# Optimization experiments

Hardware: AMD Instinct MI355X
Metric: run time of the kernel (lower is better)

Reference implementation:

```python
import jax, jax.numpy as jnp
import numpy as np

N_HEAD = 4
N_FEAT = 256
D_K = N_FEAT // N_HEAD


def setup_inputs() -> dict:
    key = jax.random.key(0)
    ks = jax.random.split(key, 7)
    B, T, F = 8, 2048, N_FEAT
    return {
        "query": jax.random.normal(ks[0], (B, T, F), dtype=jnp.float32),
        "key": jax.random.normal(ks[1], (B, T, F), dtype=jnp.float32),
        "value": jax.random.normal(ks[2], (B, T, F), dtype=jnp.float32),
        "mask": jax.random.randint(ks[3], (B, 1, T), 0, 2, dtype=jnp.int32),
        "W_qkv": jax.random.normal(ks[4], (3 * F, 3 * F), dtype=jnp.float32) * 0.02,
        "b_qkv": jnp.zeros((3 * F,), dtype=jnp.float32),
        "W_out": jax.random.normal(ks[5], (F, F), dtype=jnp.float32) * 0.02,
        "b_out": jnp.zeros((F,), dtype=jnp.float32),
    }


def reference(query, key, value, mask, W_qkv, b_qkv, W_out, b_out):
    B, T, F = query.shape
    H, dk = N_HEAD, D_K
    # fused QKV projection on concatenated [q; k; v]  -> (B, T, 3F)
    qkv = jnp.concatenate([query, key, value], axis=-1) @ W_qkv.T + b_qkv
    qkv = qkv.reshape(B, T, H, 3 * dk)
    q, k, v = jnp.split(qkv, 3, axis=-1)          # each (B, T, H, dk)
    q = q.transpose(0, 2, 1, 3)                    # (B, H, T, dk)
    k = k.transpose(0, 2, 1, 3)
    v = v.transpose(0, 2, 1, 3)
    scores = jnp.einsum("bhqd,bhkd->bhqk", q, k) / jnp.sqrt(jnp.float32(dk))
    # mask: (B, 1, T) -> broadcast (B, 1, 1, T); positions where mask==0 are masked
    m = (mask[:, None, :, :] == 0)
    min_val = jnp.finfo(scores.dtype).min
    scores = jnp.where(m, min_val, scores)
    attn = jax.nn.softmax(scores, axis=-1)
    attn = jnp.where(m, jnp.float32(0.0), attn)    # zero masked probs, as in torch code
    x = jnp.einsum("bhqk,bhkd->bhqd", attn, v)     # (B, H, T, dk)
    x = x.transpose(0, 2, 1, 3).reshape(B, T, H * dk)
    return x @ W_out.T + b_out
```

## Files before the change

kernel.cpp:

```cpp
#include <hip/hip_runtime.h>
#include <hip/hip_bf16.h>

#define NB 8
#define NT 2048
#define NH 4
#define NF 256
#define NTF 768
#define NM (NB * NT)

typedef unsigned short u16;
typedef unsigned int u32;
typedef unsigned long long u64;
typedef u16 u16x8 __attribute__((ext_vector_type(8)));
typedef __bf16 bf16x8 __attribute__((ext_vector_type(8)));
typedef float f32x4 __attribute__((ext_vector_type(4)));
typedef float f32x16 __attribute__((ext_vector_type(16)));

__device__ __forceinline__ u16 bf16_rne(float f) {
    union { float f; unsigned u; } x; x.f = f;
    unsigned u = x.u;
    return (u16)((u + 0x7fffu + ((u >> 16) & 1u)) >> 16);
}

__device__ __forceinline__ int swz(int row, int colB) {
    return row * 128 + (colB ^ ((row & 7) << 4));
}

__device__ __forceinline__ void glds16(const void* g, void* l) {
    __builtin_amdgcn_global_load_lds(
        (const __attribute__((address_space(1))) void*)g,
        (__attribute__((address_space(3))) void*)l, 16, 0, 0);
}

__device__ __forceinline__ u32 pkbf16(float lo, float hi) {
    union { __bf16 h2[2]; u32 u; } t;
    t.h2[0] = (__bf16)lo; t.h2[1] = (__bf16)hi;
    return t.u;
}

__device__ __forceinline__ void pl32swap(u32& a, u32& b) {
    asm("v_permlane32_swap_b32 %0, %1" : "+v"(a), "+v"(b));
}

#define mfma32(A, B, C) __builtin_amdgcn_mfma_f32_32x32x16_bf16((A), (B), (C), 0, 0, 0)

__global__ __launch_bounds__(256) void convert_all_kernel(
        const float* __restrict__ q, const float* __restrict__ k,
        const float* __restrict__ v, const float* __restrict__ wqkv,
        const float* __restrict__ wout, const int* __restrict__ mask,
        u16* __restrict__ xcat, u16* __restrict__ wqkvb,
        u16* __restrict__ woutb, float* __restrict__ maskadd) {
    int bid = blockIdx.x;
    if (bid < 6144) {
        int tid = bid * 256 + threadIdx.x;
        int row = tid / 96;
        int c8  = (tid % 96) * 8;
        const float* src; int c;
        if (c8 < NF)            { src = q; c = c8; }
        else if (c8 < 2 * NF)   { src = k; c = c8 - NF; }
        else                    { src = v; c = c8 - 2 * NF; }
        const float4* p = reinterpret_cast<const float4*>(src + (size_t)row * NF + c);
        float4 a = p[0], b = p[1];
        u16x8 o;
        o[0] = bf16_rne(a.x); o[1] = bf16_rne(a.y); o[2] = bf16_rne(a.z); o[3] = bf16_rne(a.w);
        o[4] = bf16_rne(b.x); o[5] = bf16_rne(b.y); o[6] = bf16_rne(b.z); o[7] = bf16_rne(b.w);
        *reinterpret_cast<u16x8*>(xcat + (size_t)row * NTF + c8) = o;
    } else if (bid < 6464) {
        int tid = (bid - 6144) * 256 + threadIdx.x;
        int i8 = tid * 8;
        const float* src; u16* dst; int off;
        if (i8 < NTF * NTF) { src = wqkv; dst = wqkvb; off = i8; }
        else                { src = wout; dst = woutb; off = i8 - NTF * NTF; }
        const float4* p = reinterpret_cast<const float4*>(src + off);
        float4 a = p[0], b = p[1];
        u16x8 o;
        o[0] = bf16_rne(a.x); o[1] = bf16_rne(a.y); o[2] = bf16_rne(a.z); o[3] = bf16_rne(a.w);
        o[4] = bf16_rne(b.x); o[5] = bf16_rne(b.y); o[6] = bf16_rne(b.z); o[7] = bf16_rne(b.w);
        *reinterpret_cast<u16x8*>(dst + off) = o;
    } else {
        int i = (bid - 6464) * 2048 + threadIdx.x * 8;
        int4 m0 = *reinterpret_cast<const int4*>(mask + i);
        int4 m1 = *reinterpret_cast<const int4*>(mask + i + 4);
        float4 f0 = { m0.x ? 0.f : -1e30f, m0.y ? 0.f : -1e30f,
                      m0.z ? 0.f : -1e30f, m0.w ? 0.f : -1e30f };
        float4 f1 = { m1.x ? 0.f : -1e30f, m1.y ? 0.f : -1e30f,
                      m1.z ? 0.f : -1e30f, m1.w ? 0.f : -1e30f };
        *reinterpret_cast<float4*>(maskadd + i) = f0;
        *reinterpret_cast<float4*>(maskadd + i + 4) = f1;
    }
}

template<int N, int K, int MODE>
__global__ __launch_bounds__(256) void gemm_kernel(
        const u16* __restrict__ A, const u16* __restrict__ Bw,
        const float* __restrict__ bias, void* __restrict__ Cout,
        u16* __restrict__ Vt) {
    __shared__ alignas(16) char smem[32768];
    char* As = smem;
    char* Bs = smem + 16384;
    int m0 = blockIdx.x * 64, n0 = blockIdx.y * 64;
    int tid = threadIdx.x;
    int w = tid >> 6, lane = tid & 63, l15 = lane & 15, hi = lane >> 4;
    int r0 = tid >> 3, cb0 = (tid & 7) * 16;
    int gcb = cb0 ^ ((r0 & 7) << 4);
    int wo = w * 1024;

    const char* Ac = (const char*)A;
    const char* Bc = (const char*)Bw;
    const char* ga0 = Ac + (size_t)(m0 + r0) * (K * 2) + gcb;
    const char* ga1 = ga0 + (size_t)32 * (K * 2);
    const char* gb0 = Bc + (size_t)(n0 + r0) * (K * 2) + gcb;
    const char* gb1 = gb0 + (size_t)32 * (K * 2);

    glds16(ga0, As + wo); glds16(ga1, As + 4096 + wo);
    glds16(gb0, Bs + wo); glds16(gb1, Bs + 4096 + wo);

    f32x4 acc[4];
#pragma unroll
    for (int ct = 0; ct < 4; ++ct) acc[ct] = (f32x4){0.f, 0.f, 0.f, 0.f};

    constexpr int NKT = K / 64;
    for (int kt = 0; kt < NKT; ++kt) {
        int cur = kt & 1;
        __syncthreads();
        if (kt + 1 < NKT) {
            int off = (kt + 1) * 128;
            char* Ad = As + (cur ^ 1) * 8192;
            char* Bd = Bs + (cur ^ 1) * 8192;
            glds16(ga0 + off, Ad + wo); glds16(ga1 + off, Ad + 4096 + wo);
            glds16(gb0 + off, Bd + wo); glds16(gb1 + off, Bd + 4096 + wo);
        }
        const char* Ax = As + cur * 8192;
        const char* Bx = Bs + cur * 8192;
#pragma unroll
        for (int ks = 0; ks < 2; ++ks) {
            bf16x8 af = *reinterpret_cast<const bf16x8*>(Ax + swz(w * 16 + l15, hi * 16 + ks * 64));
#pragma unroll
            for (int ct = 0; ct < 4; ++ct) {
                bf16x8 bf = *reinterpret_cast<const bf16x8*>(Bx + swz(ct * 16 + l15, hi * 16 + ks * 64));
                acc[ct] = __builtin_amdgcn_mfma_f32_16x16x32_bf16(af, bf, acc[ct], 0, 0, 0);
            }
        }
    }

    int orow = m0 + w * 16 + hi * 4;
    if (MODE == 2 && ((n0 >> 6) % 3) == 2) {
        int b = orow >> 11, t = orow & (NT - 1);
        int bh = b * NH + (n0 / 192);
#pragma unroll
        for (int ct = 0; ct < 4; ++ct) {
            int d = ct * 16 + l15;
            float bv = bias[n0 + d];
            union { u16 h4[4]; u64 u; } pk;
#pragma unroll
            for (int r = 0; r < 4; ++r) pk.h4[r] = bf16_rne(acc[ct][r] + bv);
            *reinterpret_cast<u64*>(Vt + (size_t)(bh * 64 + d) * NT + t) = pk.u;
        }
    } else {
#pragma unroll
        for (int ct = 0; ct < 4; ++ct) {
            int col = n0 + ct * 16 + l15;
            float bv = bias[col];
#pragma unroll
            for (int r = 0; r < 4; ++r) {
                float val = acc[ct][r] + bv;
                if (MODE == 1)
                    reinterpret_cast<float*>(Cout)[(size_t)(orow + r) * N + col] = val;
                else
                    reinterpret_cast<u16*>(Cout)[(size_t)(orow + r) * N + col] = bf16_rne(val);
            }
        }
    }
}

__global__ __launch_bounds__(512, 4) void attn_kernel(
        const u16* __restrict__ qkv, const u16* __restrict__ vt,
        const float* __restrict__ maskadd, u16* __restrict__ xout) {
    int bh = blockIdx.x;
    int q0 = blockIdx.y * 128;
    int b = bh >> 2, h = bh & 3;
    __shared__ alignas(16) char smem[65536];
    int tid = threadIdx.x;
    int w = tid >> 6, lane = tid & 63;
    int l31 = lane & 31, hv = lane >> 5;
    int wq = w & 3, g = w >> 2;
    int r0 = tid >> 3, cb0 = (tid & 7) * 16;
    int gcb = cb0 ^ ((r0 & 7) << 4);
    int wo = w * 1024;
    const float SCALE = 0.125f * 1.44269504088896340736f;

    const char* qkvC = (const char*)qkv;
    const char* vtC  = (const char*)vt;
    const char* gk0 = qkvC + (size_t)(b * NT + r0) * 1536 + h * 384 + 128 + gcb;
    const char* gv0 = vtC + (size_t)(bh * 64 + r0) * (NT * 2) + gcb;

    glds16(gk0,         smem + wo);
    glds16(gk0 + 98304, smem + 8192 + wo);
    glds16(gv0,         smem + 32768 + wo);
    glds16(gv0 + 128,   smem + 32768 + 8192 + wo);

    const char* qrow = qkvC + (size_t)(b * NT + q0 + wq * 32 + l31) * 1536
                       + h * 384 + hv * 16;
    bf16x8 bQ0 = *reinterpret_cast<const bf16x8*>(qrow);
    bf16x8 bQ1 = *reinterpret_cast<const bf16x8*>(qrow + 32);
    bf16x8 bQ2 = *reinterpret_cast<const bf16x8*>(qrow + 64);
    bf16x8 bQ3 = *reinterpret_cast<const bf16x8*>(qrow + 96);

    f32x16 accO0 = 0.f, accO1 = 0.f;
    float ssum = 0.f;
    const float* gm = maskadd + (size_t)b * NT;

    for (int j = 0; j < 16; ++j) {
        int cur = j & 1;
        __syncthreads();
        if (j < 15) {
            int tn = 2 * (j + 1);
            char* Kd = smem + (cur ^ 1) * 16384;
            char* Vd = smem + 32768 + (cur ^ 1) * 16384;
            glds16(gk0 + (size_t)tn * 98304, Kd + wo);
            glds16(gk0 + (size_t)(tn + 1) * 98304, Kd + 8192 + wo);
            glds16(gv0 + (size_t)tn * 128, Vd + wo);
            glds16(gv0 + (size_t)(tn + 1) * 128, Vd + 8192 + wo);
        }
        int t = 2 * j + g;
        const char* Kx = smem + g * 8192 + cur * 16384;
        const char* Vx = smem + 32768 + g * 8192 + cur * 16384;

        f32x16 s0 = 0.f, s1 = 0.f;
        __builtin_amdgcn_s_setprio(1);
#pragma unroll
        for (int ks = 0; ks < 4; ++ks) {
            bf16x8 a0 = *reinterpret_cast<const bf16x8*>(Kx + swz(l31, ks * 32 + hv * 16));
            bf16x8 a1 = *reinterpret_cast<const bf16x8*>(Kx + swz(32 + l31, ks * 32 + hv * 16));
            bf16x8 bq = (ks == 0) ? bQ0 : (ks == 1) ? bQ1 : (ks == 2) ? bQ2 : bQ3;
            s0 = mfma32(a0, bq, s0);
            s1 = mfma32(a1, bq, s1);
        }
        __builtin_amdgcn_s_setprio(0);

        const float* mt = gm + t * 64;
#pragma unroll
        for (int rq = 0; rq < 4; ++rq) {
            f32x4 md0 = *reinterpret_cast<const f32x4*>(mt + rq * 8 + 4 * hv);
            f32x4 md1 = *reinterpret_cast<const f32x4*>(mt + 32 + rq * 8 + 4 * hv);
#pragma unroll
            for (int e = 0; e < 4; ++e) {
                s0[rq * 4 + e] = __builtin_amdgcn_exp2f(
                    __builtin_fmaf(s0[rq * 4 + e], SCALE, md0[e]));
                s1[rq * 4 + e] = __builtin_amdgcn_exp2f(
                    __builtin_fmaf(s1[rq * 4 + e], SCALE, md1[e]));
            }
        }
        {
            f32x16 rv = s0 + s1;
            union { f32x16 v; f32x4 q[4]; } u; u.v = rv;
            f32x4 r4 = (u.q[0] + u.q[1]) + (u.q[2] + u.q[3]);
            ssum += (r4[0] + r4[1]) + (r4[2] + r4[3]);
        }

        u32 pka0[4], pkb0[4], pka1[4], pkb1[4];
#pragma unroll
        for (int rq = 0; rq < 4; ++rq) {
            pka0[rq] = pkbf16(s0[rq * 4 + 0], s0[rq * 4 + 1]);
            pkb0[rq] = pkbf16(s0[rq * 4 + 2], s0[rq * 4 + 3]);
            pka1[rq] = pkbf16(s1[rq * 4 + 0], s1[rq * 4 + 1]);
            pkb1[rq] = pkbf16(s1[rq * 4 + 2], s1[rq * 4 + 3]);
        }
        __builtin_amdgcn_s_setprio(1);
#pragma unroll
        for (int s4 = 0; s4 < 4; ++s4) {
            const int kb = s4 >> 1, sp = (s4 & 1) * 2;
            u32 B0, B1, B2, B3;
            if (kb == 0) { B0 = pka0[sp]; B2 = pka0[sp + 1]; B1 = pkb0[sp]; B3 = pkb0[sp + 1]; }
            else         { B0 = pka1[sp]; B2 = pka1[sp + 1]; B1 = pkb1[sp]; B3 = pkb1[sp + 1]; }
            pl32swap(B0, B2);
            pl32swap(B1, B3);
            union { u32 u4[4]; bf16x8 v; } bp;
            bp.u4[0] = B0; bp.u4[1] = B1; bp.u4[2] = B2; bp.u4[3] = B3;
            bf16x8 av0 = *reinterpret_cast<const bf16x8*>(Vx + swz(l31, s4 * 32 + hv * 16));
            bf16x8 av1 = *reinterpret_cast<const bf16x8*>(Vx + swz(32 + l31, s4 * 32 + hv * 16));
            accO0 = mfma32(av0, bp.v, accO0);
            accO1 = mfma32(av1, bp.v, accO1);
        }
        __builtin_amdgcn_s_setprio(0);
    }

    ssum += __shfl_xor(ssum, 32, 64);
    __syncthreads();
    float* sS = reinterpret_cast<float*>(smem + 32768);
    if (g == 1) {
        union { f32x16 v; f32x4 q[4]; } o0, o1; o0.v = accO0; o1.v = accO1;
#pragma unroll
        for (int i = 0; i < 4; ++i) {
            *reinterpret_cast<f32x4*>(smem + wq * 8192 + i * 1024 + lane * 16) = o0.q[i];
            *reinterpret_cast<f32x4*>(smem + wq * 8192 + (4 + i) * 1024 + lane * 16) = o1.q[i];
        }
        if (lane < 32) sS[wq * 32 + l31] = ssum;
    }
    __syncthreads();
    if (g == 0) {
        union { f32x16 v; f32x4 q[4]; } o0, o1; o0.v = accO0; o1.v = accO1;
#pragma unroll
        for (int i = 0; i < 4; ++i) {
            o0.q[i] += *reinterpret_cast<const f32x4*>(smem + wq * 8192 + i * 1024 + lane * 16);
            o1.q[i] += *reinterpret_cast<const f32x4*>(smem + wq * 8192 + (4 + i) * 1024 + lane * 16);
        }
        float stot = ssum + sS[wq * 32 + l31];
        float inv = stot > 0.f ? 1.0f / stot : 0.0f;
        int qg = b * NT + q0 + wq * 32 + l31;
#pragma unroll
        for (int db = 0; db < 2; ++db) {
            const float* of = db ? (const float*)&o1.v : (const float*)&o0.v;
#pragma unroll
            for (int rq = 0; rq < 4; ++rq) {
                u32 lo = pkbf16(of[rq * 4 + 0] * inv, of[rq * 4 + 1] * inv);
                u32 hi2 = pkbf16(of[rq * 4 + 2] * inv, of[rq * 4 + 3] * inv);
                u64 pk = (u64)lo | ((u64)hi2 << 32);
                int d = db * 32 + rq * 8 + 4 * hv;
                *reinterpret_cast<u64*>(xout + (size_t)qg * NF + h * 64 + d) = pk;
            }
        }
    }
}

extern "C" void kernel_launch(void* const* d_in, const int* in_sizes, int n_in,
                              void* d_out, int out_size, void* d_ws, size_t ws_size,
                              hipStream_t stream) {
    const float* q    = (const float*)d_in[0];
    const float* k    = (const float*)d_in[1];
    const float* v    = (const float*)d_in[2];
    const int*   mask = (const int*)d_in[3];
    const float* wqkv = (const float*)d_in[4];
    const float* bqkv = (const float*)d_in[5];
    const float* wout = (const float*)d_in[6];
    const float* bout = (const float*)d_in[7];
    float* out = (float*)d_out;

    char* ws = (char*)d_ws;
    u16*   Xcat    = (u16*)(ws);
    u16*   QKV     = (u16*)(ws + 25165824);
    u16*   Vt      = (u16*)(ws + 50331648);
    u16*   Xattn   = (u16*)(ws + 58720256);
    u16*   Wqkvb   = (u16*)(ws + 67108864);
    u16*   Woutb   = (u16*)(ws + 68288512);
    float* Maskadd = (float*)(ws + 68419584);

    convert_all_kernel<<<6472, 256, 0, stream>>>(q, k, v, wqkv, wout, mask,
                                                 Xcat, Wqkvb, Woutb, Maskadd);
    gemm_kernel<NTF, NTF, 2><<<dim3(NM / 64, NTF / 64), 256, 0, stream>>>(
        Xcat, Wqkvb, bqkv, QKV, Vt);
    attn_kernel<<<dim3(NB * NH, NT / 128), 512, 0, stream>>>(QKV, Vt, Maskadd, Xattn);
    gemm_kernel<NF, NF, 1><<<dim3(NM / 64, NF / 64), 256, 0, stream>>>(
        Xattn, Woutb, bout, out, nullptr);
}
```

Measured before the change: 104.4 us.

## Use 128x128 tiled GEMM kernel for fused QKV projection

Adds a dedicated QKV projection kernel with 128x128 output tiles and 4 waves, each computing a 64x64 sub-tile as a 4x4 grid of 16x16 MFMAs. The previous version used 64x64 tiles. Larger tiles raise arithmetic intensity and cut redundant global/LDS loads of the A and B operands. The cost is 64KB of LDS and more accumulator registers per block, which lowers occupancy, and fewer blocks (768). The output GEMM is simplified to an fp32-only template.

```diff
diff --git a/kernel.cpp b/kernel.cpp
--- a/kernel.cpp
+++ b/kernel.cpp
@@ -42,6 +42,7 @@
     asm("v_permlane32_swap_b32 %0, %1" : "+v"(a), "+v"(b));
 }
 
+#define mfma16(A, B, C) __builtin_amdgcn_mfma_f32_16x16x32_bf16((A), (B), (C), 0, 0, 0)
 #define mfma32(A, B, C) __builtin_amdgcn_mfma_f32_32x32x16_bf16((A), (B), (C), 0, 0, 0)
 
 __global__ __launch_bounds__(256) void convert_all_kernel(
@@ -90,11 +91,114 @@
     }
 }
 
-template<int N, int K, int MODE>
+__global__ __launch_bounds__(256) void gemm128_qkv_kernel(
+        const u16* __restrict__ A, const u16* __restrict__ Bw,
+        const float* __restrict__ bias, u16* __restrict__ QKV,
+        u16* __restrict__ Vt) {
+    __shared__ alignas(16) char smem[65536];
+    char* As = smem;
+    char* Bs = smem + 32768;
+    constexpr int K = NTF;
+    int m0 = blockIdx.x * 128, n0 = blockIdx.y * 128;
+    int tid = threadIdx.x;
+    int w = tid >> 6, lane = tid & 63, l15 = lane & 15, hi = lane >> 4;
+    int wr = w >> 1, wc = w & 1;
+    int r0 = tid >> 3, cb0 = (tid & 7) * 16;
+    int gcb = cb0 ^ ((r0 & 7) << 4);
+    int wo = w * 1024;
+
+    const char* Ac = (const char*)A;
+    const char* Bc = (const char*)Bw;
+    const char* gA = Ac + (size_t)(m0 + r0) * (K * 2) + gcb;
+    const char* gB = Bc + (size_t)(n0 + r0) * (K * 2) + gcb;
+    const size_t rstep = (size_t)32 * (K * 2);
+
+#pragma unroll
+    for (int p = 0; p < 4; ++p) {
+        glds16(gA + p * rstep, As + p * 4096 + wo);
+        glds16(gB + p * rstep, Bs + p * 4096 + wo);
+    }
+
+    f32x4 acc[4][4];
+#pragma unroll
+    for (int fi = 0; fi < 4; ++fi)
+#pragma unroll
+        for (int fj = 0; fj < 4; ++fj) acc[fi][fj] = (f32x4){0.f, 0.f, 0.f, 0.f};
+
+    constexpr int NKT = K / 64;
+    for (int kt = 0; kt < NKT; ++kt) {
+        int cur = kt & 1;
+        __syncthreads();
+        if (kt + 1 < NKT) {
+            int off = (kt + 1) * 128;
+            char* Ad = As + (cur ^ 1) * 16384;
+            char* Bd = Bs + (cur ^ 1) * 16384;
+#pragma unroll
+            for (int p = 0; p < 4; ++p) {
+                glds16(gA + p * rstep + off, Ad + p * 4096 + wo);
+                glds16(gB + p * rstep + off, Bd + p * 4096 + wo);
+            }
+        }
+        const char* Ax = As + cur * 16384;
+        const char* Bx = Bs + cur * 16384;
+#pragma unroll
+        for (int ks = 0; ks < 2; ++ks) {
+            bf16x8 af[4], bf[4];
+#pragma unroll
+            for (int fi = 0; fi < 4; ++fi)
+                af[fi] = *reinterpret_cast<const bf16x8*>(
+                    Ax + swz(wr * 64 + fi * 16 + l15, hi * 16 + ks * 64));
+#pragma unroll
+            for (int fj = 0; fj < 4; ++fj)
+                bf[fj] = *reinterpret_cast<const bf16x8*>(
+                    Bx + swz(wc * 64 + fj * 16 + l15, hi * 16 + ks * 64));
+#pragma unroll
+            for (int fi = 0; fi < 4; ++fi)
+#pragma unroll
+                for (int fj = 0; fj < 4; ++fj)
+                    acc[fi][fj] = mfma16(af[fi], bf[fj], acc[fi][fj]);
+        }
+    }
+
+    int g64 = (n0 >> 6) + wc;
+    int typ = g64 % 3, h = g64 / 3;
+    int rowBase = m0 + wr * 64;
+    if (typ == 2) {
+        int b = rowBase >> 11;
+        int bh = b * NH + h;
+#pragma unroll
+        for (int fi = 0; fi < 4; ++fi) {
+            int t = (rowBase + fi * 16 + hi * 4) & (NT - 1);
+#pragma unroll
+            for (int fj = 0; fj < 4; ++fj) {
+                int d = fj * 16 + l15;
+                float bv = bias[n0 + wc * 64 + d];
+                u32 lo = pkbf16(acc[fi][fj][0] + bv, acc[fi][fj][1] + bv);
+                u32 hi2 = pkbf16(acc[fi][fj][2] + bv, acc[fi][fj][3] + bv);
+                u64 pk = (u64)lo | ((u64)hi2 << 32);
+                *reinterpret_cast<u64*>(Vt + (size_t)(bh * 64 + d) * NT + t) = pk;
+            }
+        }
+    } else {
+#pragma unroll
+        for (int fi = 0; fi < 4; ++fi) {
+            int orow = rowBase + fi * 16 + hi * 4;
+#pragma unroll
+            for (int fj = 0; fj < 4; ++fj) {
+                int col = n0 + wc * 64 + fj * 16 + l15;
+                float bv = bias[col];
+#pragma unroll
+                for (int r = 0; r < 4; ++r)
+                    QKV[(size_t)(orow + r) * NTF + col] = bf16_rne(acc[fi][fj][r] + bv);
+            }
+        }
+    }
+}
+
+template<int N, int K>
 __global__ __launch_bounds__(256) void gemm_kernel(
         const u16* __restrict__ A, const u16* __restrict__ Bw,
-        const float* __restrict__ bias, void* __restrict__ Cout,
-        u16* __restrict__ Vt) {
+        const float* __restrict__ bias, float* __restrict__ Cout) {
     __shared__ alignas(16) char smem[32768];
     char* As = smem;
     char* Bs = smem + 16384;
@@ -138,38 +242,19 @@
 #pragma unroll
             for (int ct = 0; ct < 4; ++ct) {
                 bf16x8 bf = *reinterpret_cast<const bf16x8*>(Bx + swz(ct * 16 + l15, hi * 16 + ks * 64));
-                acc[ct] = __builtin_amdgcn_mfma_f32_16x16x32_bf16(af, bf, acc[ct], 0, 0, 0);
+                acc[ct] = mfma16(af, bf, acc[ct]);
             }
         }
     }
 
     int orow = m0 + w * 16 + hi * 4;
-    if (MODE == 2 && ((n0 >> 6) % 3) == 2) {
-        int b = orow >> 11, t = orow & (NT - 1);
-        int bh = b * NH + (n0 / 192);
-#pragma unroll
-        for (int ct = 0; ct < 4; ++ct) {
-            int d = ct * 16 + l15;
-            float bv = bias[n0 + d];
-            union { u16 h4[4]; u64 u; } pk;
-#pragma unroll
-            for (int r = 0; r < 4; ++r) pk.h4[r] = bf16_rne(acc[ct][r] + bv);
-            *reinterpret_cast<u64*>(Vt + (size_t)(bh * 64 + d) * NT + t) = pk.u;
-        }
-    } else {
-#pragma unroll
-        for (int ct = 0; ct < 4; ++ct) {
-            int col = n0 + ct * 16 + l15;
-            float bv = bias[col];
-#pragma unroll
-            for (int r = 0; r < 4; ++r) {
-                float val = acc[ct][r] + bv;
-                if (MODE == 1)
-                    reinterpret_cast<float*>(Cout)[(size_t)(orow + r) * N + col] = val;
-                else
-                    reinterpret_cast<u16*>(Cout)[(size_t)(orow + r) * N + col] = bf16_rne(val);
-            }
-        }
+#pragma unroll
+    for (int ct = 0; ct < 4; ++ct) {
+        int col = n0 + ct * 16 + l15;
+        float bv = bias[col];
+#pragma unroll
+        for (int r = 0; r < 4; ++r)
+            Cout[(size_t)(orow + r) * N + col] = acc[ct][r] + bv;
     }
 }
 
@@ -347,9 +432,9 @@
 
     convert_all_kernel<<<6472, 256, 0, stream>>>(q, k, v, wqkv, wout, mask,
                                                  Xcat, Wqkvb, Woutb, Maskadd);
-    gemm_kernel<NTF, NTF, 2><<<dim3(NM / 64, NTF / 64), 256, 0, stream>>>(
+    gemm128_qkv_kernel<<<dim3(NM / 128, NTF / 128), 256, 0, stream>>>(
         Xcat, Wqkvb, bqkv, QKV, Vt);
     attn_kernel<<<dim3(NB * NH, NT / 128), 512, 0, stream>>>(QKV, Vt, Maskadd, Xattn);
-    gemm_kernel<NF, NF, 1><<<dim3(NM / 64, NF / 64), 256, 0, stream>>>(
-        Xattn, Woutb, bout, out, nullptr);
-}
+    gemm_kernel<NF, NF><<<dim3(NM / 64, NF / 64), 256, 0, stream>>>(
+        Xattn, Woutb, bout, out);
+}
```

New measurement: 101.2 us, median of 2. -3.0%, faster.
